# Optimization experiments

Hardware: AMD Instinct MI355X
Metric: run time of the kernel (lower is better)

Reference implementation:

```python
import jax, jax.numpy as jnp
import numpy as np

L, B = 1024, 256
IN_DIM, AUX_DIM, OUT_DIM = 64, 32, 128
GATE_DIM = AUX_DIM + OUT_DIM  # gates see [xa, normalized c] only


def setup_inputs() -> dict:
    key = jax.random.key(0)
    ks = jax.random.split(key, 5)
    return {
        "xm": jax.random.uniform(ks[0], (L, B, IN_DIM), dtype=jnp.float32),
        "xa": jax.random.normal(ks[1], (L, B, AUX_DIM), dtype=jnp.float32),
        "W_r": jax.random.normal(ks[2], (OUT_DIM * OUT_DIM, GATE_DIM), dtype=jnp.float32) * 0.05,
        "b_r": jnp.zeros((OUT_DIM * OUT_DIM,), dtype=jnp.float32),
        "W_i": jax.random.normal(ks[3], (IN_DIM * OUT_DIM, GATE_DIM), dtype=jnp.float32) * 0.05,
        "b_i": jnp.zeros((IN_DIM * OUT_DIM,), dtype=jnp.float32),
        "W_o": jax.random.normal(ks[4], (OUT_DIM, GATE_DIM), dtype=jnp.float32) * 0.05,
        "b_o": jnp.full((OUT_DIM,), -3.0, dtype=jnp.float32),
    }


def reference(xm, xa, W_r, b_r, W_i, b_i, W_o, b_o):
    def step(c, inp):
        xm_t, xa_t = inp  # (B, IN_DIM), (B, AUX_DIM)
        c_sum = jnp.sum(c, axis=-1, keepdims=True)
        scale = jnp.where(c_sum == 0, jnp.ones_like(c_sum), c_sum)
        g = jnp.concatenate([xa_t, c / scale], axis=-1)  # (B, GATE_DIM)
        r = jax.nn.softmax((g @ W_r.T + b_r).reshape(-1, OUT_DIM, OUT_DIM), axis=-1)
        i = jax.nn.softmax((g @ W_i.T + b_i).reshape(-1, IN_DIM, OUT_DIM), axis=-1)
        o = jax.nn.sigmoid(g @ W_o.T + b_o)  # (B, OUT_DIM)
        c_new = jnp.einsum("bo,bop->bp", c, r) + jnp.einsum("bi,bio->bo", xm_t, i)
        h = o * c_new
        return c_new - h, (h, c_new - h)

    c0 = jnp.zeros((xm.shape[1], OUT_DIM), dtype=xm.dtype)
    _, (hs, cs) = jax.lax.scan(step, c0, (xm, xa))
    return hs, cs
```

## Files before the change

kernel.cpp:

```cpp
#include <hip/hip_runtime.h>


#define LSTEPS 1024
#define LOG2E 1.4426950408889634f

typedef unsigned short u16;
typedef unsigned int u32;
typedef unsigned long long u64;
typedef __attribute__((ext_vector_type(8))) short s8v;
typedef __attribute__((ext_vector_type(4))) float f4v;

__device__ u32 cnt_mem[4 * 2 * 64];
__device__ float bank_mem[2u * 4 * 64 * 64 * 128];
__device__ float c2pub[2 * 256 * 128];

static __device__ __forceinline__ u16 f2bf(float f) {
  u32 u = __float_as_uint(f);
  u += 0x7fffu + ((u >> 16) & 1u);
  return (u16)(u >> 16);
}

template <typename T>
static __device__ __forceinline__ T ldc(const T* p) {
  return __hip_atomic_load(p, __ATOMIC_RELAXED, __HIP_MEMORY_SCOPE_AGENT);
}
template <typename T>
static __device__ __forceinline__ void stc(T* p, T v) {
  __hip_atomic_store(p, v, __ATOMIC_RELAXED, __HIP_MEMORY_SCOPE_AGENT);
}

static __device__ __forceinline__ void lds_bar() {
  asm volatile("s_waitcnt lgkmcnt(0)" ::: "memory");
  __builtin_amdgcn_s_barrier();
  __builtin_amdgcn_sched_barrier(0);
}
static __device__ __forceinline__ void wait_cnt(u32* c, u32 target) {
  if (threadIdx.x == 0) {
    while (__hip_atomic_load(c, __ATOMIC_RELAXED, __HIP_MEMORY_SCOPE_AGENT) < target)
      __builtin_amdgcn_s_sleep(2);
  }
  __builtin_amdgcn_s_barrier();
  __builtin_amdgcn_sched_barrier(0);
}
static __device__ __forceinline__ void arrive_wait(u32* c, u32 target) {
  asm volatile("s_waitcnt vmcnt(0)" ::: "memory");
  __builtin_amdgcn_s_barrier();
  if (threadIdx.x == 0) {
    __hip_atomic_fetch_add(c, 1u, __ATOMIC_RELAXED, __HIP_MEMORY_SCOPE_AGENT);
    while (__hip_atomic_load(c, __ATOMIC_RELAXED, __HIP_MEMORY_SCOPE_AGENT) < target)
      __builtin_amdgcn_s_sleep(2);
  }
  __builtin_amdgcn_s_barrier();
  __builtin_amdgcn_sched_barrier(0);
}

__global__ __launch_bounds__(256) void convert_w_kernel(
    const float* __restrict__ Wr, const float* __restrict__ Wi, const float* __restrict__ Wo,
    u16* __restrict__ WrB, u16* __restrict__ WiB, u16* __restrict__ WoB) {
  if (blockIdx.x == 0)
    for (int i = threadIdx.x; i < 4 * 2 * 64; i += 256) cnt_mem[i] = 0;
  const int n1 = 16384 * 160, n2 = 8192 * 160, n3 = 128 * 160;
  const int stride = gridDim.x * blockDim.x;
  int idx = blockIdx.x * blockDim.x + threadIdx.x;
  for (; idx < n1 + n2 + n3; idx += stride) {
    if (idx < n1)            WrB[idx]           = f2bf(Wr[idx] * LOG2E);
    else if (idx < n1 + n2)  WiB[idx - n1]      = f2bf(Wi[idx - n1] * LOG2E);
    else                     WoB[idx - n1 - n2] = f2bf(Wo[idx - n1 - n2] * (-LOG2E));
  }
}

__global__ __launch_bounds__(512, 1) void persist_kernel(
    const float* __restrict__ xm, const float* __restrict__ xa,
    const float* __restrict__ br, const float* __restrict__ bi, const float* __restrict__ bo,
    const u16* __restrict__ WrB, const u16* __restrict__ WiB, const u16* __restrict__ WoB,
    float* __restrict__ o_buf,
    float* __restrict__ hs_out, float* __restrict__ cs_out) {
  __shared__ u16 W_lds[3][128][168];
  __shared__ u16 g_lds[64][168];
  __shared__ float zex[3][64][4];
  __shared__ float c_col[3][64];
  __shared__ float xm_col[3][64];
  __shared__ float red[4][128];

  const int tid = threadIdx.x;
  const int wg = blockIdx.x;
  const int xcd = wg & 7;
  const int l32 = wg >> 3;
  const int btile = l32 & 3;
  const int oslot = l32 >> 2;
  const int rank = oslot * 8 + xcd;
  const int orow0 = xcd * 24 + oslot * 3;
  u32* scnt = cnt_mem + (btile * 2 + 0) * 64;
  u32* ccnt = cnt_mem + (btile * 2 + 1) * 64;

  const int lane = tid & 63;
  const int wv = tid >> 6;
  const int wm = wv >> 2;
  const int wn = wv & 3;
  const int lg = lane >> 4;
  const int lc = lane & 15;

#pragma unroll
  for (int rb = 0; rb < 3; ++rb) {
    const int orow = orow0 + rb;
    const u16* wbp = (orow < 128) ? (WrB + (size_t)orow * 20480)
                                  : (WiB + (size_t)(orow - 128) * 20480);
#pragma unroll
    for (int i = 0; i < 5; ++i) {
      const int chunk = tid + i * 512;
      uint4 v = ((const uint4*)wbp)[chunk];
      *(uint4*)((char*)&W_lds[rb][0][0] + (chunk / 20) * 336 + (chunk % 20) * 16) = v;
    }
  }
  float biasA[3], biasB[3];
#pragma unroll
  for (int task = 0; task < 3; ++task) {
    const int orow = orow0 + task;
    const float* bptr = (orow < 128) ? (br + orow * 128) : (bi + (orow - 128) * 128);
    biasA[task] = bptr[wn * 32 + lc] * LOG2E;
    biasB[task] = bptr[wn * 32 + 16 + lc] * LOG2E;
  }
  const bool duty = (oslot < 4) && (xcd == ((oslot + 2 * btile) & 7)) && (wn == 0);
  const int qoff = (oslot & 3) * 32;
  const float ob0 = bo[qoff + lc] * (-LOG2E);
  const float ob1 = bo[qoff + 16 + lc] * (-LOG2E);

  const int bloc = tid >> 3;
  const int seg = tid & 7;
  const int pseg = seg * 16;
  const int bg = btile * 64 + bloc;

  for (int t = 0; t <= LSTEPS; ++t) {
    f4v xa4 = (f4v){0.f, 0.f, 0.f, 0.f};
    float xmv = 0.f;
    if (t < LSTEPS) {
      xa4 = ((const f4v*)(xa + ((size_t)t * 256 + bg) * 32))[seg];
      if (tid < 192) {
        const int col0 = orow0 + (tid >> 6);
        if (col0 >= 128)
          xmv = xm[((size_t)t * 256 + btile * 64 + (tid & 63)) * 64 + (col0 - 128)];
      }
    }

    if (t) wait_cnt(scnt, 64u * (u32)t);

    const int p = tid & 127;
    float olog = 0.f;

    if (t > 0) {
      const float* B = bank_mem + (size_t)((t - 1) & 1) * 2097152 +
                       (size_t)btile * 524288 + (size_t)rank * 128;
      const int bgi = tid >> 7;
      float s = 0.f;
#pragma unroll
      for (int k = 0; k < 16; ++k) s += ldc(B + (size_t)(bgi * 16 + k) * 8192 + p);
      red[bgi][p] = s;
      if (tid < 128)
        olog = ldc(o_buf + ((t - 1) & 1) * 32768 + (btile * 64 + rank) * 128 + p);
    }
    lds_bar();
    if (t > 0 && tid < 128) {
      float cn = red[0][p] + red[1][p] + red[2][p] + red[3][p];
      float e2 = __builtin_amdgcn_exp2f(olog);
      float og = __builtin_amdgcn_rcpf(1.f + e2);
      float h = og * cn;
      float c2 = cn - h;
      hs_out[((size_t)(t - 1) * 256 + btile * 64 + rank) * 128 + p] = h;
      cs_out[((size_t)(t - 1) * 256 + btile * 64 + rank) * 128 + p] = c2;
      stc(c2pub + (t & 1) * 32768 + (btile * 64 + rank) * 128 + p, c2);
    }
    if (t == LSTEPS) break;

    if (t) arrive_wait(ccnt, 64u * (u32)t);

    if (t > 0) {
      const float* ca = c2pub + (t & 1) * 32768 + bg * 128 + pseg;
      f4v cv4[4];
#pragma unroll
      for (int q = 0; q < 4; ++q)
        asm volatile("global_load_dwordx4 %0, %1, off sc0 sc1"
                     : "=v"(cv4[q]) : "v"(ca + q * 4) : "memory");
      asm volatile("s_waitcnt vmcnt(0)"
                   : "+v"(cv4[0]), "+v"(cv4[1]), "+v"(cv4[2]), "+v"(cv4[3])
                   :: "memory");
      float cc[16];
      float csum = 0.f;
#pragma unroll
      for (int q = 0; q < 4; ++q)
#pragma unroll
        for (int j = 0; j < 4; ++j) {
          cc[q * 4 + j] = cv4[q][j];
          csum += cv4[q][j];
        }
      csum += __shfl_xor(csum, 1);
      csum += __shfl_xor(csum, 2);
      csum += __shfl_xor(csum, 4);
      const float sc = (csum == 0.f) ? 1.f : csum;
      const float inv = __builtin_amdgcn_rcpf(sc);
      u32 w[8];
#pragma unroll
      for (int k = 0; k < 8; ++k)
        w[k] = (u32)f2bf(cc[2 * k] * inv) | ((u32)f2bf(cc[2 * k + 1] * inv) << 16);
      uint4* gdst = (uint4*)&g_lds[bloc][32 + pseg];
      gdst[0] = make_uint4(w[0], w[1], w[2], w[3]);
      gdst[1] = make_uint4(w[4], w[5], w[6], w[7]);
    } else {
      uint4* gdst = (uint4*)&g_lds[bloc][32 + pseg];
      gdst[0] = make_uint4(0, 0, 0, 0);
      gdst[1] = make_uint4(0, 0, 0, 0);
    }

    {
      uint2 pk = make_uint2((u32)f2bf(xa4[0]) | ((u32)f2bf(xa4[1]) << 16),
                            (u32)f2bf(xa4[2]) | ((u32)f2bf(xa4[3]) << 16));
      *(uint2*)&g_lds[bloc][seg * 4] = pk;
    }

    if (tid < 192) {
      const int task = tid >> 6, bl = tid & 63;
      const int col0 = orow0 + task;
      if (col0 < 128) {
        c_col[task][bl] = (t > 0)
            ? ldc(c2pub + (t & 1) * 32768 + (btile * 64 + bl) * 128 + col0) : 0.f;
      } else {
        xm_col[task][bl] = xmv;
      }
    }
    lds_bar();

    s8v afr[2][5];
#pragma unroll
    for (int mt = 0; mt < 2; ++mt)
#pragma unroll
      for (int ks = 0; ks < 5; ++ks)
        afr[mt][ks] = *(const s8v*)&g_lds[wm * 32 + mt * 16 + lc][ks * 32 + lg * 8];

    if (duty) {
      f4v oacc[2][2];
#pragma unroll
      for (int mt = 0; mt < 2; ++mt) {
        oacc[mt][0] = (f4v){ob0, ob0, ob0, ob0};
        oacc[mt][1] = (f4v){ob1, ob1, ob1, ob1};
      }
#pragma unroll
      for (int ks = 0; ks < 5; ++ks) {
        s8v b0 = *(const s8v*)(WoB + (size_t)(qoff + lc) * 160 + ks * 32 + lg * 8);
        s8v b1 = *(const s8v*)(WoB + (size_t)(qoff + 16 + lc) * 160 + ks * 32 + lg * 8);
        oacc[0][0] = __builtin_amdgcn_mfma_f32_16x16x32_bf16(afr[0][ks], b0, oacc[0][0], 0, 0, 0);
        oacc[1][0] = __builtin_amdgcn_mfma_f32_16x16x32_bf16(afr[1][ks], b0, oacc[1][0], 0, 0, 0);
        oacc[0][1] = __builtin_amdgcn_mfma_f32_16x16x32_bf16(afr[0][ks], b1, oacc[0][1], 0, 0, 0);
        oacc[1][1] = __builtin_amdgcn_mfma_f32_16x16x32_bf16(afr[1][ks], b1, oacc[1][1], 0, 0, 0);
      }
      float* ob = o_buf + (t & 1) * 32768;
#pragma unroll
      for (int mt = 0; mt < 2; ++mt)
#pragma unroll
        for (int nt = 0; nt < 2; ++nt)
#pragma unroll
          for (int r = 0; r < 4; ++r)
            stc(&ob[(btile * 64 + wm * 32 + mt * 16 + lg * 4 + r) * 128 + qoff + nt * 16 + lc],
                oacc[mt][nt][r]);
    }

    float cpart[2][2][4] = {};

#pragma unroll
    for (int task = 0; task < 3; ++task) {
      const int orow = orow0 + task;
      const bool is_r = (orow < 128);
      f4v acc[2][2];
#pragma unroll
      for (int mt = 0; mt < 2; ++mt) {
        acc[mt][0] = (f4v){biasA[task], biasA[task], biasA[task], biasA[task]};
        acc[mt][1] = (f4v){biasB[task], biasB[task], biasB[task], biasB[task]};
      }
#pragma unroll
      for (int ks = 0; ks < 5; ++ks) {
        s8v b0 = *(const s8v*)&W_lds[task][wn * 32 + lc][ks * 32 + lg * 8];
        s8v b1 = *(const s8v*)&W_lds[task][wn * 32 + 16 + lc][ks * 32 + lg * 8];
        acc[0][0] = __builtin_amdgcn_mfma_f32_16x16x32_bf16(afr[0][ks], b0, acc[0][0], 0, 0, 0);
        acc[1][0] = __builtin_amdgcn_mfma_f32_16x16x32_bf16(afr[1][ks], b0, acc[1][0], 0, 0, 0);
        acc[0][1] = __builtin_amdgcn_mfma_f32_16x16x32_bf16(afr[0][ks], b1, acc[0][1], 0, 0, 0);
        acc[1][1] = __builtin_amdgcn_mfma_f32_16x16x32_bf16(afr[1][ks], b1, acc[1][1], 0, 0, 0);
      }
      float ev[2][2][4];
      float zp[2][4];
#pragma unroll
      for (int mt = 0; mt < 2; ++mt)
#pragma unroll
        for (int r = 0; r < 4; ++r) {
          float e0 = __builtin_amdgcn_exp2f(acc[mt][0][r]);
          float e1 = __builtin_amdgcn_exp2f(acc[mt][1][r]);
          ev[mt][0][r] = e0;
          ev[mt][1][r] = e1;
          zp[mt][r] = e0 + e1;
        }
#pragma unroll
      for (int mt = 0; mt < 2; ++mt)
#pragma unroll
        for (int r = 0; r < 4; ++r) {
          float z = zp[mt][r];
          z += __shfl_xor(z, 1);
          z += __shfl_xor(z, 2);
          z += __shfl_xor(z, 4);
          z += __shfl_xor(z, 8);
          zp[mt][r] = z;
        }
      if (lc == 0) {
#pragma unroll
        for (int mt = 0; mt < 2; ++mt)
          *(float4*)&zex[task][(wm * 4 + wn) * 8 + mt * 4 + lg][0] =
              make_float4(zp[mt][0], zp[mt][1], zp[mt][2], zp[mt][3]);
      }
      lds_bar();
#pragma unroll
      for (int mt = 0; mt < 2; ++mt) {
        float Z[4] = {0.f, 0.f, 0.f, 0.f};
#pragma unroll
        for (int w2 = 0; w2 < 4; ++w2) {
          float4 v = *(const float4*)&zex[task][(wm * 4 + w2) * 8 + mt * 4 + lg][0];
          Z[0] += v.x; Z[1] += v.y; Z[2] += v.z; Z[3] += v.w;
        }
#pragma unroll
        for (int r = 0; r < 4; ++r) {
          const int brow = wm * 32 + mt * 16 + lg * 4 + r;
          const float cv = is_r ? c_col[task][brow] : xm_col[task][brow];
          const float coef = cv * __builtin_amdgcn_rcpf(Z[r]);
          cpart[mt][0][r] += coef * ev[mt][0][r];
          cpart[mt][1][r] += coef * ev[mt][1][r];
        }
      }
    }

    {
      float* bb = bank_mem + (size_t)(t & 1) * 2097152 + (size_t)btile * 524288 +
                  (size_t)rank * 8192;
      const int q1 = lc & 1;
      const int pq0 = wn * 32 + (lc & ~1);
#pragma unroll
      for (int mt = 0; mt < 2; ++mt)
#pragma unroll
        for (int nt = 0; nt < 2; ++nt) {
          float a0 = cpart[mt][nt][0], a1 = cpart[mt][nt][1];
          float a2 = cpart[mt][nt][2], a3 = cpart[mt][nt][3];
          float t0 = __shfl_xor(a0, 1), t1 = __shfl_xor(a1, 1);
          float t2 = __shfl_xor(a2, 1), t3 = __shfl_xor(a3, 1);
          float b0 = q1 ? t1 : a0;
          float b1 = q1 ? a1 : t0;
          float b2 = q1 ? t3 : a2;
          float b3 = q1 ? a3 : t2;
          const int r1 = wm * 32 + mt * 16 + lg * 4 + q1;
          const int pq = pq0 + nt * 16;
          u64 pk1 = (u64)__float_as_uint(b0) | ((u64)__float_as_uint(b1) << 32);
          u64 pk2 = (u64)__float_as_uint(b2) | ((u64)__float_as_uint(b3) << 32);
          stc((u64*)(bb + (size_t)r1 * 128 + pq), pk1);
          stc((u64*)(bb + (size_t)(r1 + 2) * 128 + pq), pk2);
        }
    }

    asm volatile("s_waitcnt vmcnt(0)" ::: "memory");
    __builtin_amdgcn_s_barrier();
    __builtin_amdgcn_sched_barrier(0);
    if (tid == 0)
      __hip_atomic_fetch_add(scnt, 1u, __ATOMIC_RELAXED, __HIP_MEMORY_SCOPE_AGENT);
  }
}

__global__ __launch_bounds__(512, 2) void step_kernel(
    const float* __restrict__ xm, const float* __restrict__ xa,
    const float* __restrict__ br, const float* __restrict__ bi, const float* __restrict__ bo,
    const u16* __restrict__ WrB, const u16* __restrict__ WiB, const u16* __restrict__ WoB,
    float* __restrict__ c_acc, float* __restrict__ o_buf,
    float* __restrict__ hs_out, float* __restrict__ cs_out, int t) {
  __shared__ u16 W_lds[128][168];
  __shared__ u16 g_lds[64][160];

  const int tid = threadIdx.x;
  const int wg = blockIdx.x;
  const int xcd = wg & 7;
  const int l32 = wg >> 3;
  const int btile = l32 & 3;
  const int oslot = l32 >> 2;
  const int rank = oslot * 8 + xcd;
  const int orow0 = xcd * 24 + oslot * 3;

  const int lane = tid & 63;
  const int wv = tid >> 6;
  const int wm = wv >> 2;
  const int wn = wv & 3;
  const int lg = lane >> 4;
  const int lc = lane & 15;

  if (t < LSTEPS && tid < 32) {
    float4* zb = (float4*)(c_acc + ((t + 1) % 3) * 32768 + wg * 128);
    zb[tid] = make_float4(0.f, 0.f, 0.f, 0.f);
  }

  const int bloc = tid >> 3;
  const int seg = tid & 7;
  const int pseg = seg * 16;
  const int bg = btile * 64 + bloc;

  if (t > 0) {
    const float* ca = c_acc + ((t + 2) % 3) * 32768 + bg * 128 + pseg;
    const float* ol = o_buf + ((t + 1) & 1) * 32768 + bg * 128 + pseg;
    float hv[16], cc[16];
    float csum = 0.f;
#pragma unroll
    for (int q = 0; q < 4; ++q) {
      float4 cn = ((const float4*)ca)[q];
      float4 sl = ((const float4*)ol)[q];
      float cna[4] = {cn.x, cn.y, cn.z, cn.w};
      float sla[4] = {sl.x, sl.y, sl.z, sl.w};
#pragma unroll
      for (int j = 0; j < 4; ++j) {
        float e2 = __builtin_amdgcn_exp2f(sla[j]);
        float og = __builtin_amdgcn_rcpf(1.f + e2);
        float h = og * cna[j];
        float c2 = cna[j] - h;
        hv[q * 4 + j] = h;
        cc[q * 4 + j] = c2;
        csum += c2;
      }
    }
    csum += __shfl_xor(csum, 1);
    csum += __shfl_xor(csum, 2);
    csum += __shfl_xor(csum, 4);
    float sc = (csum == 0.f) ? 1.f : csum;
    float inv = __builtin_amdgcn_rcpf(sc);
    if (bloc == rank) {
      float* ho = hs_out + ((size_t)(t - 1) * 256 + bg) * 128 + pseg;
      float* co = cs_out + ((size_t)(t - 1) * 256 + bg) * 128 + pseg;
#pragma unroll
      for (int q = 0; q < 4; ++q) {
        ((float4*)ho)[q] = make_float4(hv[q * 4], hv[q * 4 + 1], hv[q * 4 + 2], hv[q * 4 + 3]);
        ((float4*)co)[q] = make_float4(cc[q * 4], cc[q * 4 + 1], cc[q * 4 + 2], cc[q * 4 + 3]);
      }
    }
    u32 w[8];
#pragma unroll
    for (int k = 0; k < 8; ++k)
      w[k] = (u32)f2bf(cc[2 * k] * inv) | ((u32)f2bf(cc[2 * k + 1] * inv) << 16);
    uint4* gdst = (uint4*)&g_lds[bloc][32 + pseg];
    gdst[0] = make_uint4(w[0], w[1], w[2], w[3]);
    gdst[1] = make_uint4(w[4], w[5], w[6], w[7]);
  } else {
    uint4* gdst = (uint4*)&g_lds[bloc][32 + pseg];
    gdst[0] = make_uint4(0, 0, 0, 0);
    gdst[1] = make_uint4(0, 0, 0, 0);
  }

  if (t == LSTEPS) return;

  {
    float4 xv = ((const float4*)(xa + ((size_t)t * 256 + bg) * 32))[seg];
    uint2 pk = make_uint2((u32)f2bf(xv.x) | ((u32)f2bf(xv.y) << 16),
                          (u32)f2bf(xv.z) | ((u32)f2bf(xv.w) << 16));
    *(uint2*)&g_lds[bloc][seg * 4] = pk;
  }
  __syncthreads();

  s8v afr[2][5];
#pragma unroll
  for (int mt = 0; mt < 2; ++mt)
#pragma unroll
    for (int ks = 0; ks < 5; ++ks)
      afr[mt][ks] = *(const s8v*)&g_lds[wm * 32 + mt * 16 + lc][ks * 32 + lg * 8];

  float cpart[2][2][4] = {};
  const float* cprev = c_acc + ((t + 2) % 3) * 32768;
  const float* oprev = o_buf + ((t + 1) & 1) * 32768;

  uint4 pf[5];
  {
    const u16* wbp = (orow0 < 128) ? (WrB + (size_t)orow0 * 20480)
                                   : (WiB + (size_t)(orow0 - 128) * 20480);
#pragma unroll
    for (int i = 0; i < 5; ++i) pf[i] = ((const uint4*)wbp)[tid + i * 512];
  }
#pragma unroll
  for (int i = 0; i < 5; ++i) {
    int chunk = tid + i * 512;
    *(uint4*)((char*)&W_lds[0][0] + (chunk / 20) * 336 + (chunk % 20) * 16) = pf[i];
  }
  __syncthreads();

  for (int task = 0; task < 3; ++task) {
    const int orow = orow0 + task;
    const bool is_r = (orow < 128);
    if (task < 2) {
      const int nr = orow + 1;
      const u16* wbp = (nr < 128) ? (WrB + (size_t)nr * 20480)
                                  : (WiB + (size_t)(nr - 128) * 20480);
#pragma unroll
      for (int i = 0; i < 5; ++i) pf[i] = ((const uint4*)wbp)[tid + i * 512];
    }
    const float* bptr = is_r ? (br + orow * 128) : (bi + (orow - 128) * 128);
    float bias0 = bptr[wn * 32 + lc] * LOG2E;
    float bias1 = bptr[wn * 32 + 16 + lc] * LOG2E;
    f4v acc[2][2];
#pragma unroll
    for (int mt = 0; mt < 2; ++mt) {
      acc[mt][0] = (f4v){bias0, bias0, bias0, bias0};
      acc[mt][1] = (f4v){bias1, bias1, bias1, bias1};
    }
#pragma unroll
    for (int ks = 0; ks < 5; ++ks) {
      s8v b0 = *(const s8v*)&W_lds[wn * 32 + lc][ks * 32 + lg * 8];
      s8v b1 = *(const s8v*)&W_lds[wn * 32 + 16 + lc][ks * 32 + lg * 8];
      acc[0][0] = __builtin_amdgcn_mfma_f32_16x16x32_bf16(afr[0][ks], b0, acc[0][0], 0, 0, 0);
      acc[1][0] = __builtin_amdgcn_mfma_f32_16x16x32_bf16(afr[1][ks], b0, acc[1][0], 0, 0, 0);
      acc[0][1] = __builtin_amdgcn_mfma_f32_16x16x32_bf16(afr[0][ks], b1, acc[0][1], 0, 0, 0);
      acc[1][1] = __builtin_amdgcn_mfma_f32_16x16x32_bf16(afr[1][ks], b1, acc[1][1], 0, 0, 0);
    }
    float ev[2][2][4];
    float zp[2][4];
#pragma unroll
    for (int mt = 0; mt < 2; ++mt)
#pragma unroll
      for (int r = 0; r < 4; ++r) {
        float e0 = __builtin_amdgcn_exp2f(acc[mt][0][r]);
        float e1 = __builtin_amdgcn_exp2f(acc[mt][1][r]);
        ev[mt][0][r] = e0;
        ev[mt][1][r] = e1;
        zp[mt][r] = e0 + e1;
      }
#pragma unroll
    for (int mt = 0; mt < 2; ++mt)
#pragma unroll
      for (int r = 0; r < 4; ++r) {
        float z = zp[mt][r];
        z += __shfl_xor(z, 1);
        z += __shfl_xor(z, 2);
        z += __shfl_xor(z, 4);
        z += __shfl_xor(z, 8);
        zp[mt][r] = z;
      }
    if (lc == 0) {
#pragma unroll
      for (int mt = 0; mt < 2; ++mt)
        *(float4*)((char*)&W_lds[0][0] + ((wm * 4 + wn) * 8 + mt * 4 + lg) * 336 + 320) =
            make_float4(zp[mt][0], zp[mt][1], zp[mt][2], zp[mt][3]);
    }
    __syncthreads();
#pragma unroll
    for (int mt = 0; mt < 2; ++mt) {
      float Z[4] = {0.f, 0.f, 0.f, 0.f};
#pragma unroll
      for (int w2 = 0; w2 < 4; ++w2) {
        float4 v = *(const float4*)((char*)&W_lds[0][0] + ((wm * 4 + w2) * 8 + mt * 4 + lg) * 336 + 320);
        Z[0] += v.x; Z[1] += v.y; Z[2] += v.z; Z[3] += v.w;
      }
#pragma unroll
      for (int r = 0; r < 4; ++r) {
        const int brow = wm * 32 + mt * 16 + lg * 4 + r;
        const int bg2 = btile * 64 + brow;
        float cv;
        if (is_r) {
          if (t > 0) {
            float cn = cprev[bg2 * 128 + orow];
            float s2 = oprev[bg2 * 128 + orow];
            float e2 = __builtin_amdgcn_exp2f(s2);
            cv = cn * e2 * __builtin_amdgcn_rcpf(1.f + e2);
          } else cv = 0.f;
        } else {
          cv = xm[((size_t)t * 256 + bg2) * 64 + (orow - 128)];
        }
        float coef = cv * __builtin_amdgcn_rcpf(Z[r]);
        cpart[mt][0][r] += coef * ev[mt][0][r];
        cpart[mt][1][r] += coef * ev[mt][1][r];
      }
    }
    if (task < 2) {
#pragma unroll
      for (int i = 0; i < 5; ++i) {
        int chunk = tid + i * 512;
        *(uint4*)((char*)&W_lds[0][0] + (chunk / 20) * 336 + (chunk % 20) * 16) = pf[i];
      }
      __syncthreads();
    }
  }

  if (oslot < 4 && xcd == ((oslot + 2 * btile) & 7) && wn == 0) {
    const int qoff = oslot * 32;
    float ob0 = bo[qoff + lc] * (-LOG2E);
    float ob1 = bo[qoff + 16 + lc] * (-LOG2E);
    f4v oacc[2][2];
#pragma unroll
    for (int mt = 0; mt < 2; ++mt) {
      oacc[mt][0] = (f4v){ob0, ob0, ob0, ob0};
      oacc[mt][1] = (f4v){ob1, ob1, ob1, ob1};
    }
#pragma unroll
    for (int ks = 0; ks < 5; ++ks) {
      s8v b0 = *(const s8v*)(WoB + (size_t)(qoff + lc) * 160 + ks * 32 + lg * 8);
      s8v b1 = *(const s8v*)(WoB + (size_t)(qoff + 16 + lc) * 160 + ks * 32 + lg * 8);
      oacc[0][0] = __builtin_amdgcn_mfma_f32_16x16x32_bf16(afr[0][ks], b0, oacc[0][0], 0, 0, 0);
      oacc[1][0] = __builtin_amdgcn_mfma_f32_16x16x32_bf16(afr[1][ks], b0, oacc[1][0], 0, 0, 0);
      oacc[0][1] = __builtin_amdgcn_mfma_f32_16x16x32_bf16(afr[0][ks], b1, oacc[0][1], 0, 0, 0);
      oacc[1][1] = __builtin_amdgcn_mfma_f32_16x16x32_bf16(afr[1][ks], b1, oacc[1][1], 0, 0, 0);
    }
    float* ob = o_buf + (t & 1) * 32768;
#pragma unroll
    for (int mt = 0; mt < 2; ++mt)
#pragma unroll
      for (int nt = 0; nt < 2; ++nt)
#pragma unroll
        for (int r = 0; r < 4; ++r)
          ob[(btile * 64 + wm * 32 + mt * 16 + lg * 4 + r) * 128 + qoff + nt * 16 + lc] = oacc[mt][nt][r];
  }

  float* cb = c_acc + (t % 3) * 32768;
#pragma unroll
  for (int mt = 0; mt < 2; ++mt)
#pragma unroll
    for (int nt = 0; nt < 2; ++nt)
#pragma unroll
      for (int r = 0; r < 4; ++r)
        unsafeAtomicAdd(&cb[(btile * 64 + wm * 32 + mt * 16 + lg * 4 + r) * 128 + wn * 32 + nt * 16 + lc],
                        cpart[mt][nt][r]);
}

extern "C" void kernel_launch(void* const* d_in, const int* in_sizes, int n_in,
                              void* d_out, int out_size, void* d_ws, size_t ws_size,
                              hipStream_t stream) {
  const float* xm = (const float*)d_in[0];
  const float* xa = (const float*)d_in[1];
  const float* Wr = (const float*)d_in[2];
  const float* br = (const float*)d_in[3];
  const float* Wi = (const float*)d_in[4];
  const float* bi = (const float*)d_in[5];
  const float* Wo = (const float*)d_in[6];
  const float* bo = (const float*)d_in[7];

  if (ws_size < 8560640) return;
  u16* WrB = (u16*)d_ws;
  u16* WiB = WrB + 16384 * 160;
  u16* WoB = WiB + 8192 * 160;
  float* c_acc = (float*)(WoB + 128 * 160);
  float* o_buf = c_acc + 3 * 32768;

  float* hs = (float*)d_out;
  float* cs = hs + (size_t)LSTEPS * 256 * 128;

  convert_w_kernel<<<dim3(1024), dim3(256), 0, stream>>>(Wr, Wi, Wo, WrB, WiB, WoB);
  (void)hipMemsetAsync(c_acc, 0, 3 * 32768 * sizeof(float), stream);

  void* kargs[] = {(void*)&xm, (void*)&xa, (void*)&br, (void*)&bi, (void*)&bo,
                   (void*)&WrB, (void*)&WiB, (void*)&WoB,
                   (void*)&o_buf, (void*)&hs, (void*)&cs};
  hipError_t st = hipLaunchCooperativeKernel((const void*)persist_kernel, dim3(256), dim3(512),
                                             kargs, 0, stream);
  if (st != hipSuccess) {
    for (int t = 0; t <= LSTEPS; ++t)
      step_kernel<<<dim3(256), dim3(512), 0, stream>>>(xm, xa, br, bi, bo, WrB, WiB, WoB,
                                                       c_acc, o_buf, hs, cs, t);
  }
}
```

Baseline: 17.50 ms.

## Split grid barrier counters per oslot and defer hs/cs stores past barrier

Replaces the single per-btile atomic counter, which 64 workgroups all increment, with 8 padded counters, one per oslot. Eight lanes poll them in parallel, and the sleep interval is shortened to cut contention on one cache line. The hs/cs output stores are moved after the compute phase so they no longer sit on the critical path before the arrive barrier, where their vmcnt wait would hold it up. The cost is more polling loads and more counter memory.

```diff
diff --git a/kernel.cpp b/kernel.cpp
--- a/kernel.cpp
+++ b/kernel.cpp
@@ -10,7 +10,7 @@
 typedef __attribute__((ext_vector_type(8))) short s8v;
 typedef __attribute__((ext_vector_type(4))) float f4v;
 
-__device__ u32 cnt_mem[4 * 2 * 64];
+__device__ u32 cnt_mem[4 * 2 * 8 * 64];
 __device__ float bank_mem[2u * 4 * 64 * 64 * 128];
 __device__ float c2pub[2 * 256 * 128];
 
@@ -34,21 +34,24 @@
   __builtin_amdgcn_s_barrier();
   __builtin_amdgcn_sched_barrier(0);
 }
-static __device__ __forceinline__ void wait_cnt(u32* c, u32 target) {
-  if (threadIdx.x == 0) {
-    while (__hip_atomic_load(c, __ATOMIC_RELAXED, __HIP_MEMORY_SCOPE_AGENT) < target)
-      __builtin_amdgcn_s_sleep(2);
+static __device__ __forceinline__ void wait_cnt8(u32* c, u32 target) {
+  if (threadIdx.x < 8) {
+    while (__hip_atomic_load(c + threadIdx.x * 64, __ATOMIC_RELAXED,
+                             __HIP_MEMORY_SCOPE_AGENT) < target)
+      __builtin_amdgcn_s_sleep(1);
   }
   __builtin_amdgcn_s_barrier();
   __builtin_amdgcn_sched_barrier(0);
 }
-static __device__ __forceinline__ void arrive_wait(u32* c, u32 target) {
+static __device__ __forceinline__ void arrive_wait8(u32* c, int oslot, u32 target) {
   asm volatile("s_waitcnt vmcnt(0)" ::: "memory");
   __builtin_amdgcn_s_barrier();
-  if (threadIdx.x == 0) {
-    __hip_atomic_fetch_add(c, 1u, __ATOMIC_RELAXED, __HIP_MEMORY_SCOPE_AGENT);
-    while (__hip_atomic_load(c, __ATOMIC_RELAXED, __HIP_MEMORY_SCOPE_AGENT) < target)
-      __builtin_amdgcn_s_sleep(2);
+  if (threadIdx.x == 0)
+    __hip_atomic_fetch_add(c + oslot * 64, 1u, __ATOMIC_RELAXED, __HIP_MEMORY_SCOPE_AGENT);
+  if (threadIdx.x < 8) {
+    while (__hip_atomic_load(c + threadIdx.x * 64, __ATOMIC_RELAXED,
+                             __HIP_MEMORY_SCOPE_AGENT) < target)
+      __builtin_amdgcn_s_sleep(1);
   }
   __builtin_amdgcn_s_barrier();
   __builtin_amdgcn_sched_barrier(0);
@@ -58,7 +61,7 @@
     const float* __restrict__ Wr, const float* __restrict__ Wi, const float* __restrict__ Wo,
     u16* __restrict__ WrB, u16* __restrict__ WiB, u16* __restrict__ WoB) {
   if (blockIdx.x == 0)
-    for (int i = threadIdx.x; i < 4 * 2 * 64; i += 256) cnt_mem[i] = 0;
+    for (int i = threadIdx.x; i < 4 * 2 * 8 * 64; i += 256) cnt_mem[i] = 0;
   const int n1 = 16384 * 160, n2 = 8192 * 160, n3 = 128 * 160;
   const int stride = gridDim.x * blockDim.x;
   int idx = blockIdx.x * blockDim.x + threadIdx.x;
@@ -90,8 +93,8 @@
   const int oslot = l32 >> 2;
   const int rank = oslot * 8 + xcd;
   const int orow0 = xcd * 24 + oslot * 3;
-  u32* scnt = cnt_mem + (btile * 2 + 0) * 64;
-  u32* ccnt = cnt_mem + (btile * 2 + 1) * 64;
+  u32* scnt = cnt_mem + (btile * 2 + 0) * 8 * 64;
+  u32* ccnt = cnt_mem + (btile * 2 + 1) * 8 * 64;
 
   const int lane = tid & 63;
   const int wv = tid >> 6;
@@ -142,10 +145,10 @@
       }
     }
 
-    if (t) wait_cnt(scnt, 64u * (u32)t);
+    if (t) wait_cnt8(scnt, 8u * (u32)t);
 
     const int p = tid & 127;
-    float olog = 0.f;
+    float olog = 0.f, hOut = 0.f, c2Out = 0.f;
 
     if (t > 0) {
       const float* B = bank_mem + (size_t)((t - 1) & 1) * 2097152 +
@@ -163,15 +166,19 @@
       float cn = red[0][p] + red[1][p] + red[2][p] + red[3][p];
       float e2 = __builtin_amdgcn_exp2f(olog);
       float og = __builtin_amdgcn_rcpf(1.f + e2);
-      float h = og * cn;
-      float c2 = cn - h;
-      hs_out[((size_t)(t - 1) * 256 + btile * 64 + rank) * 128 + p] = h;
-      cs_out[((size_t)(t - 1) * 256 + btile * 64 + rank) * 128 + p] = c2;
-      stc(c2pub + (t & 1) * 32768 + (btile * 64 + rank) * 128 + p, c2);
-    }
-    if (t == LSTEPS) break;
-
-    if (t) arrive_wait(ccnt, 64u * (u32)t);
+      hOut = og * cn;
+      c2Out = cn - hOut;
+      stc(c2pub + (t & 1) * 32768 + (btile * 64 + rank) * 128 + p, c2Out);
+    }
+    if (t == LSTEPS) {
+      if (tid < 128) {
+        hs_out[((size_t)(t - 1) * 256 + btile * 64 + rank) * 128 + p] = hOut;
+        cs_out[((size_t)(t - 1) * 256 + btile * 64 + rank) * 128 + p] = c2Out;
+      }
+      break;
+    }
+
+    if (t) arrive_wait8(ccnt, oslot, 8u * (u32)t);
 
     if (t > 0) {
       const float* ca = c2pub + (t & 1) * 32768 + bg * 128 + pseg;
@@ -330,6 +337,11 @@
           cpart[mt][1][r] += coef * ev[mt][1][r];
         }
       }
+    }
+
+    if (t > 0 && tid < 128) {
+      hs_out[((size_t)(t - 1) * 256 + btile * 64 + rank) * 128 + p] = hOut;
+      cs_out[((size_t)(t - 1) * 256 + btile * 64 + rank) * 128 + p] = c2Out;
     }
 
     {
@@ -362,7 +374,7 @@
     __builtin_amdgcn_s_barrier();
     __builtin_amdgcn_sched_barrier(0);
     if (tid == 0)
-      __hip_atomic_fetch_add(scnt, 1u, __ATOMIC_RELAXED, __HIP_MEMORY_SCOPE_AGENT);
+      __hip_atomic_fetch_add(scnt + oslot * 64, 1u, __ATOMIC_RELAXED, __HIP_MEMORY_SCOPE_AGENT);
   }
 }
 
```

Result: faster. 15.46 ms (-11.7%).
